# Kernel tuning notes

Measured on AMD Instinct MI355X. Metric: run time of the kernel, lower is better.

The kernel has to match this reference:

```python
import jax, jax.numpy as jnp
import numpy as np

EPS = 1e-12  # torch F.normalize eps


def setup_inputs() -> dict:
    key = jax.random.key(0)
    k1, k2, k3 = jax.random.split(key, 3)
    b, c, h, w = 4, 192, 128, 128
    num_heads = 8
    in1 = jax.random.normal(k1, (b, c, h, w), dtype=jnp.float32)
    in2 = jax.random.normal(k2, (b, c, h, w), dtype=jnp.float32)
    scale = jnp.ones((num_heads, 1, 1), dtype=jnp.float32)
    proj_w = jax.random.normal(k3, (c, c), dtype=jnp.float32) * (1.0 / np.sqrt(c))
    return {"in1": in1, "in2": in2, "scale": scale, "proj_w": proj_w, "num_heads": num_heads}


def reference(in1, in2, scale, proj_w, num_heads):
    b, c, h, w = in1.shape
    hd = c // num_heads
    hw = h * w
    # b (head c) h w -> b head c (h w)
    q = in1.reshape(b, num_heads, hd, hw)
    k = in2.reshape(b, num_heads, hd, hw)
    # L2-normalize along the (h w) axis, torch eps semantics
    q = q / jnp.maximum(jnp.linalg.norm(q, axis=-1, keepdims=True), EPS)
    k = k / jnp.maximum(jnp.linalg.norm(k, axis=-1, keepdims=True), EPS)
    # channel-wise attention: [b, head, c, c]
    attn = jnp.einsum('bhcn,bhdn->bhcd', q, k) * scale  # scale broadcasts [head,1,1]
    attn = jax.nn.softmax(attn, axis=-1)
    out = jnp.einsum('bhcd,bhdn->bhcn', attn, k)
    out = out.reshape(b, c, h, w)
    # 1x1 conv projection (no bias)
    out = jnp.einsum('oc,bchw->bohw', proj_w, out)
    return out
```

## Files before the change

kernel.cpp:

```cpp
#include <hip/hip_runtime.h>
#include <hip/hip_bf16.h>
#include <math.h>

#define BATCH 4
#define NHEAD 8
#define HD 24
#define CH 192
#define HW 16384
#define SPL 64
#define SROW 640

#define OFF_MO (32 * SPL * SROW)

#define LSTR 132

typedef __attribute__((ext_vector_type(8)))  short bf16x8;
typedef __attribute__((ext_vector_type(16))) float f32x16;

__device__ __forceinline__ unsigned short bf16rne(float x) {
    union { float f; unsigned u; } v; v.f = x;
    unsigned u = v.u;
    return (unsigned short)((u + 0x7FFFu + ((u >> 16) & 1u)) >> 16);
}

__device__ __forceinline__ unsigned pack2(float a, float b) {
    union { __hip_bfloat162 h; unsigned u; } c;
    c.h = __float22bfloat162_rn(float2{a, b});
    return c.u;
}

__global__ __launch_bounds__(256, 4) void kA(const float* __restrict__ q,
                                             const float* __restrict__ k,
                                             float* __restrict__ ws) {
    __shared__ unsigned int tile[2][HD * LSTR];

    const int bh   = blockIdx.x;
    const int ch   = blockIdx.y;
    const int t    = threadIdx.x;
    const int lane = t & 63;
    const int wave = t >> 6;
    const int m    = lane & 31;
    const int hi   = lane >> 5;

    const float* qb = q + (size_t)bh * HD * HW + ch * 256;
    const float* kb = k + (size_t)bh * HD * HW + ch * 256;

    #pragma unroll
    for (int j = 0; j < 6; ++j) {
        const int idx = j * 256 + t;
        const int row = idx >> 6;
        const int c64 = idx & 63;
        float4 qv = *(const float4*)(qb + (size_t)row * HW + c64 * 4);
        float4 kv = *(const float4*)(kb + (size_t)row * HW + c64 * 4);
        *(uint2*)&tile[0][row * LSTR + c64 * 2] = make_uint2(pack2(qv.x, qv.y), pack2(qv.z, qv.w));
        *(uint2*)&tile[1][row * LSTR + c64 * 2] = make_uint2(pack2(kv.x, kv.y), pack2(kv.z, kv.w));
    }
    __syncthreads();

    const int rowc = (m < HD) ? m : 0;
    f32x16 aQK = {}, aQQ = {}, aKK = {};
    #pragma unroll
    for (int s = 0; s < 4; ++s) {
        const int off = (wave * 64 + s * 16) >> 1;
        bf16x8 aq = *(const bf16x8*)&tile[0][rowc * LSTR + off + hi * 4];
        bf16x8 bk = *(const bf16x8*)&tile[1][rowc * LSTR + off + hi * 4];
        aQK = __builtin_amdgcn_mfma_f32_32x32x16_bf16(aq, bk, aQK, 0, 0, 0);
        aQQ = __builtin_amdgcn_mfma_f32_32x32x16_bf16(aq, aq, aQQ, 0, 0, 0);
        aKK = __builtin_amdgcn_mfma_f32_32x32x16_bf16(bk, bk, aKK, 0, 0, 0);
    }
    __syncthreads();

    float* red = (float*)tile;
    if (m < HD) {
        #pragma unroll
        for (int r = 0; r < 16; ++r) {
            const int i = (r & 3) + 8 * (r >> 2) + 4 * hi;
            if (i < HD) {
                red[wave * 624 + i * HD + m] = aQK[r];
                if (i == m) {
                    red[wave * 624 + 576 + i] = aQQ[r];
                    red[wave * 624 + 600 + i] = aKK[r];
                }
            }
        }
    }
    __syncthreads();

    float* Srow = ws + ((size_t)bh * SPL + ch) * SROW;
    for (int e = t; e < 624; e += 256)
        Srow[e] = red[e] + red[624 + e] + red[1248 + e] + red[1872 + e];
}

__global__ __launch_bounds__(256) void kB(const float* __restrict__ scale,
                                          const float* __restrict__ w,
                                          float* __restrict__ ws,
                                          unsigned short* __restrict__ Mo) {
    const int bh = blockIdx.x;
    const int b  = bh >> 3;
    const int h  = bh & 7;
    const int t  = threadIdx.x;

    __shared__ float SA[624];
    __shared__ float qinv[HD], kinv[HD];
    __shared__ float wl[CH * HD];

    const float* base = ws + (size_t)bh * SPL * SROW;

    float a0 = 0.f, a1 = 0.f, a2 = 0.f;
    const int e0 = t, e1 = t + 256, e2 = t + 512;
    for (int sp = 0; sp < SPL; ++sp) {
        const float* r = base + (size_t)sp * SROW;
        a0 += r[e0];
        a1 += r[e1];
        if (t < 112) a2 += r[e2];
    }
    SA[e0] = a0; SA[e1] = a1;
    if (t < 112) SA[e2] = a2;

    for (int idx = t; idx < CH * HD; idx += 256) {
        int o = idx / HD, dd = idx % HD;
        wl[idx] = w[o * CH + h * HD + dd];
    }
    __syncthreads();

    if (t < 2 * HD) {
        float s = SA[576 + t];
        float inv = 1.0f / fmaxf(sqrtf(s), 1e-12f);
        if (t < HD) qinv[t] = inv; else kinv[t - HD] = inv;
    }
    __syncthreads();

    const float sc = scale[h];
    for (int e = t; e < HD * HD; e += 256)
        SA[e] = SA[e] * qinv[e / HD] * kinv[e % HD] * sc;
    __syncthreads();

    if (t < HD) {
        float m = -1e30f;
        for (int j = 0; j < HD; ++j) m = fmaxf(m, SA[t * HD + j]);
        float sum = 0.f;
        for (int j = 0; j < HD; ++j) {
            float v = expf(SA[t * HD + j] - m);
            SA[t * HD + j] = v;
            sum += v;
        }
        float r = 1.0f / sum;
        for (int j = 0; j < HD; ++j) SA[t * HD + j] *= r;
    }
    __syncthreads();

    for (int idx = t; idx < CH * HD; idx += 256) {
        int o = idx / HD, j = idx % HD;
        float v = 0.f;
        #pragma unroll
        for (int i = 0; i < HD; ++i) v = fmaf(wl[o * HD + i], SA[i * HD + j], v);
        Mo[(size_t)b * CH * CH + (size_t)o * CH + h * HD + j] = bf16rne(v * kinv[j]);
    }
}

#define KCN 64
#define BSTR 20

__global__ __launch_bounds__(256, 4) void kC(const float* __restrict__ k,
                                             const unsigned short* __restrict__ Mo,
                                             float* __restrict__ out) {
    __shared__ unsigned int Bt[KCN * BSTR];

    const int t    = threadIdx.x;
    const int lane = t & 63;
    const int wave = t >> 6;
    const int n31  = lane & 31;
    const int hi   = lane >> 5;
    const int nt   = wave & 1;
    const int otb  = (wave >> 1) * 3;

    const int nb = blockIdx.x * KCN;
    const int b  = blockIdx.y;

    const float* kb = k + (size_t)b * CH * HW;
    const unsigned short* Mob = Mo + (size_t)b * CH * CH;

    const int sn = t & 63;
    const int cq = t >> 6;

    f32x16 acc[3] = {};

    for (int c0 = 0; c0 < CH; c0 += 32) {
        if (c0) __syncthreads();
        float v[8];
        #pragma unroll
        for (int cc = 0; cc < 8; ++cc)
            v[cc] = kb[(size_t)(c0 + cq * 8 + cc) * HW + nb + sn];
        unsigned int wd[4];
        #pragma unroll
        for (int g = 0; g < 4; ++g) wd[g] = pack2(v[2 * g], v[2 * g + 1]);
        *(uint2*)&Bt[sn * BSTR + cq * 4]     = make_uint2(wd[0], wd[1]);
        *(uint2*)&Bt[sn * BSTR + cq * 4 + 2] = make_uint2(wd[2], wd[3]);
        __syncthreads();

        #pragma unroll
        for (int kc = 0; kc < 2; ++kc) {
            bf16x8 Bf = *(const bf16x8*)&Bt[(nt * 32 + n31) * BSTR + kc * 8 + hi * 4];
            #pragma unroll
            for (int oi = 0; oi < 3; ++oi) {
                const unsigned short* ap =
                    Mob + (size_t)((otb + oi) * 32 + n31) * CH + c0 + kc * 16 + hi * 8;
                bf16x8 Af = *(const bf16x8*)ap;
                acc[oi] = __builtin_amdgcn_mfma_f32_32x32x16_bf16(Af, Bf, acc[oi], 0, 0, 0);
            }
        }
    }

    float* op = out + (size_t)b * CH * HW;
    const int n = nb + nt * 32 + n31;
    #pragma unroll
    for (int oi = 0; oi < 3; ++oi)
        #pragma unroll
        for (int r = 0; r < 16; ++r) {
            int o = (otb + oi) * 32 + (r & 3) + 8 * (r >> 2) + 4 * hi;
            op[(size_t)o * HW + n] = acc[oi][r];
        }
}

extern "C" void kernel_launch(void* const* d_in, const int* in_sizes, int n_in,
                              void* d_out, int out_size, void* d_ws, size_t ws_size,
                              hipStream_t stream) {
    const float* in1   = (const float*)d_in[0];
    const float* in2   = (const float*)d_in[1];
    const float* scale = (const float*)d_in[2];
    const float* projw = (const float*)d_in[3];
    float* ws  = (float*)d_ws;
    float* out = (float*)d_out;
    unsigned short* Mo = (unsigned short*)(ws + OFF_MO);

    kA<<<dim3(32, SPL), 256, 0, stream>>>(in1, in2, ws);
    kB<<<32, 256, 0, stream>>>(scale, projw, ws, Mo);
    kC<<<dim3(HW / KCN, BATCH), 256, 0, stream>>>(in2, Mo, out);
}
```

Measured before the change: 194.2 us.

## Widen kB to 1024 threads and double kC channel step with float2 loads

kB now runs 1024 threads per block. Four groups each reduce a quarter of the split partial sums into shared memory, then combine them, so the serial reduction and the projection loop are shorter. kC stages 64 channels per iteration instead of 32, using float2 global loads and a wider LDS stride. This halves the number of barriers and load phases per tile and makes the global reads wider. The cost is more registers and LDS per thread in kC, which could lower occupancy.

```diff
diff --git a/kernel.cpp b/kernel.cpp
--- a/kernel.cpp
+++ b/kernel.cpp
@@ -91,15 +91,18 @@
         Srow[e] = red[e] + red[624 + e] + red[1248 + e] + red[1872 + e];
 }
 
-__global__ __launch_bounds__(256) void kB(const float* __restrict__ scale,
-                                          const float* __restrict__ w,
-                                          float* __restrict__ ws,
-                                          unsigned short* __restrict__ Mo) {
+__global__ __launch_bounds__(1024) void kB(const float* __restrict__ scale,
+                                           const float* __restrict__ w,
+                                           float* __restrict__ ws,
+                                           unsigned short* __restrict__ Mo) {
     const int bh = blockIdx.x;
     const int b  = bh >> 3;
     const int h  = bh & 7;
     const int t  = threadIdx.x;
-
+    const int g  = t >> 8;
+    const int u  = t & 255;
+
+    __shared__ float part[4][624];
     __shared__ float SA[624];
     __shared__ float qinv[HD], kinv[HD];
     __shared__ float wl[CH * HD];
@@ -107,32 +110,33 @@
     const float* base = ws + (size_t)bh * SPL * SROW;
 
     float a0 = 0.f, a1 = 0.f, a2 = 0.f;
-    const int e0 = t, e1 = t + 256, e2 = t + 512;
-    for (int sp = 0; sp < SPL; ++sp) {
+    for (int sp = g * 16; sp < g * 16 + 16; ++sp) {
         const float* r = base + (size_t)sp * SROW;
-        a0 += r[e0];
-        a1 += r[e1];
-        if (t < 112) a2 += r[e2];
-    }
-    SA[e0] = a0; SA[e1] = a1;
-    if (t < 112) SA[e2] = a2;
-
-    for (int idx = t; idx < CH * HD; idx += 256) {
+        a0 += r[u];
+        a1 += r[u + 256];
+        if (u < 112) a2 += r[u + 512];
+    }
+    part[g][u] = a0;
+    part[g][u + 256] = a1;
+    if (u < 112) part[g][u + 512] = a2;
+
+    for (int idx = t; idx < CH * HD; idx += 1024) {
         int o = idx / HD, dd = idx % HD;
         wl[idx] = w[o * CH + h * HD + dd];
     }
     __syncthreads();
 
+    if (t < 624) SA[t] = part[0][t] + part[1][t] + part[2][t] + part[3][t];
+    __syncthreads();
+
     if (t < 2 * HD) {
-        float s = SA[576 + t];
-        float inv = 1.0f / fmaxf(sqrtf(s), 1e-12f);
+        float inv = 1.0f / fmaxf(sqrtf(SA[576 + t]), 1e-12f);
         if (t < HD) qinv[t] = inv; else kinv[t - HD] = inv;
     }
     __syncthreads();
 
     const float sc = scale[h];
-    for (int e = t; e < HD * HD; e += 256)
-        SA[e] = SA[e] * qinv[e / HD] * kinv[e % HD] * sc;
+    if (t < 576) SA[t] = SA[t] * qinv[t / HD] * kinv[t % HD] * sc;
     __syncthreads();
 
     if (t < HD) {
@@ -149,7 +153,7 @@
     }
     __syncthreads();
 
-    for (int idx = t; idx < CH * HD; idx += 256) {
+    for (int idx = t; idx < CH * HD; idx += 1024) {
         int o = idx / HD, j = idx % HD;
         float v = 0.f;
         #pragma unroll
@@ -159,12 +163,13 @@
 }
 
 #define KCN 64
-#define BSTR 20
+#define CSTEP 64
+#define BSTR2 36
 
 __global__ __launch_bounds__(256, 4) void kC(const float* __restrict__ k,
                                              const unsigned short* __restrict__ Mo,
                                              float* __restrict__ out) {
-    __shared__ unsigned int Bt[KCN * BSTR];
+    __shared__ unsigned int Bt[KCN * BSTR2];
 
     const int t    = threadIdx.x;
     const int lane = t & 63;
@@ -180,27 +185,33 @@
     const float* kb = k + (size_t)b * CH * HW;
     const unsigned short* Mob = Mo + (size_t)b * CH * CH;
 
-    const int sn = t & 63;
-    const int cq = t >> 6;
+    const int np = t & 31;
+    const int cg = t >> 5;
 
     f32x16 acc[3] = {};
 
-    for (int c0 = 0; c0 < CH; c0 += 32) {
+    for (int c0 = 0; c0 < CH; c0 += CSTEP) {
         if (c0) __syncthreads();
-        float v[8];
+        float2 v[8];
         #pragma unroll
         for (int cc = 0; cc < 8; ++cc)
-            v[cc] = kb[(size_t)(c0 + cq * 8 + cc) * HW + nb + sn];
-        unsigned int wd[4];
-        #pragma unroll
-        for (int g = 0; g < 4; ++g) wd[g] = pack2(v[2 * g], v[2 * g + 1]);
-        *(uint2*)&Bt[sn * BSTR + cq * 4]     = make_uint2(wd[0], wd[1]);
-        *(uint2*)&Bt[sn * BSTR + cq * 4 + 2] = make_uint2(wd[2], wd[3]);
+            v[cc] = *(const float2*)(kb + (size_t)(c0 + cg * 8 + cc) * HW + nb + np * 2);
+        unsigned int w0[4], w1[4];
+        #pragma unroll
+        for (int g = 0; g < 4; ++g) {
+            w0[g] = pack2(v[2 * g].x, v[2 * g + 1].x);
+            w1[g] = pack2(v[2 * g].y, v[2 * g + 1].y);
+        }
+        const int n0 = np * 2;
+        *(uint2*)&Bt[n0 * BSTR2 + cg * 4]           = make_uint2(w0[0], w0[1]);
+        *(uint2*)&Bt[n0 * BSTR2 + cg * 4 + 2]       = make_uint2(w0[2], w0[3]);
+        *(uint2*)&Bt[(n0 + 1) * BSTR2 + cg * 4]     = make_uint2(w1[0], w1[1]);
+        *(uint2*)&Bt[(n0 + 1) * BSTR2 + cg * 4 + 2] = make_uint2(w1[2], w1[3]);
         __syncthreads();
 
         #pragma unroll
-        for (int kc = 0; kc < 2; ++kc) {
-            bf16x8 Bf = *(const bf16x8*)&Bt[(nt * 32 + n31) * BSTR + kc * 8 + hi * 4];
+        for (int kc = 0; kc < 4; ++kc) {
+            bf16x8 Bf = *(const bf16x8*)&Bt[(nt * 32 + n31) * BSTR2 + kc * 8 + hi * 4];
             #pragma unroll
             for (int oi = 0; oi < 3; ++oi) {
                 const unsigned short* ap =
@@ -234,6 +245,6 @@
     unsigned short* Mo = (unsigned short*)(ws + OFF_MO);
 
     kA<<<dim3(32, SPL), 256, 0, stream>>>(in1, in2, ws);
-    kB<<<32, 256, 0, stream>>>(scale, projw, ws, Mo);
+    kB<<<32, 1024, 0, stream>>>(scale, projw, ws, Mo);
     kC<<<dim3(HW / KCN, BATCH), 256, 0, stream>>>(in2, Mo, out);
 }
```

Result: faster. 176.1 us (-9.3%).
